# Kernel tuning notes

Hardware: AMD Instinct MI355X
Metric: run time of the kernel (lower is better)

Reference implementation:

```python
import jax, jax.numpy as jnp
import numpy as np

N_NODES = 50000
N_EDGES = 800000
D_IN = 128
D_HID = 128
N_LAYERS = 3
BN_EPS = 1e-5
NEG_SLOPE = 0.2  # GATv2Conv default


def setup_inputs() -> dict:
    key = jax.random.key(0)
    ks = jax.random.split(key, 9)
    x = jax.random.normal(ks[0], (N_NODES, D_IN), dtype=jnp.float32)
    edge_index = jax.random.randint(ks[1], (2, N_EDGES), 0, N_NODES, dtype=jnp.int64)
    s = 1.0 / np.sqrt(D_HID)
    # stacked per-layer params (in_channels == hidden_channels so uniform shapes)
    Wl = jax.random.uniform(ks[2], (N_LAYERS, D_IN, D_HID), jnp.float32, -s, s)   # lin_l (source)
    Wr = jax.random.uniform(ks[3], (N_LAYERS, D_IN, D_HID), jnp.float32, -s, s)   # lin_r (target)
    att = jax.random.uniform(ks[4], (N_LAYERS, D_HID), jnp.float32, -s, s)        # attention vector (heads=1)
    bias = jnp.zeros((N_LAYERS, D_HID), jnp.float32)
    gamma = jnp.ones((N_LAYERS, D_HID), jnp.float32)
    beta = jnp.zeros((N_LAYERS, D_HID), jnp.float32)
    return {"x": x, "edge_index": edge_index, "Wl": Wl, "Wr": Wr, "att": att,
            "bias": bias, "gamma": gamma, "beta": beta}


def reference(x, edge_index, Wl, Wr, att, bias, gamma, beta):
    src = edge_index[0]  # message source j
    dst = edge_index[1]  # message target i
    n = x.shape[0]
    for i in range(N_LAYERS):
        # GATv2Conv, heads=1, add_self_loops=False
        xl = x @ Wl[i]                                   # [N, H] source transform
        xr = x @ Wr[i]                                   # [N, H] target transform
        e = jax.nn.leaky_relu(xl[src] + xr[dst], NEG_SLOPE) @ att[i]  # [E]
        # softmax over incoming edges of each target node
        emax = jax.ops.segment_max(e, dst, num_segments=n)            # [N]
        a = jnp.exp(e - emax[dst])                                    # [E]
        denom = jax.ops.segment_sum(a, dst, num_segments=n)           # [N]
        alpha = a / (denom[dst] + 1e-16)                              # [E]
        out = jax.ops.segment_sum(alpha[:, None] * xl[src], dst, num_segments=n) + bias[i]
        # BatchNorm1d (training-mode batch statistics, biased variance)
        mu = jnp.mean(out, axis=0)
        var = jnp.var(out, axis=0)
        out = gamma[i] * (out - mu) * jax.lax.rsqrt(var + BN_EPS) + beta[i]
        # exact (erf) GELU to match torch F.gelu; dropout p=0.0 -> identity
        x = jax.nn.gelu(out, approximate=False)
    return x
```

## Files before the change

### kernel.cpp

```cpp
#include <hip/hip_runtime.h>
#include <math.h>

#define NNODES 50000
#define NEDGES 800000
#define D 128
#define NEG_SLOPE 0.2f
#define BN_EPS 1e-5f
#define SCAN_THREADS 1024
#define WAVE_REGION 3328
#define COUNTS_PAD (16 * WAVE_REGION)
#define SBIN 4096
#define SUM_SLOTS 64

typedef __attribute__((ext_vector_type(8))) unsigned short ushort8_t;
typedef __attribute__((ext_vector_type(8))) short bf16x8;
typedef __attribute__((ext_vector_type(4))) float f32x4;

__device__ __forceinline__ unsigned short f2bf(float x) {
  unsigned u = __float_as_uint(x);
  u += 0x7fffu + ((u >> 16) & 1u);
  return (unsigned short)(u >> 16);
}
__device__ __forceinline__ float bf2f(unsigned short h) {
  return __uint_as_float((unsigned)h << 16);
}

__global__ __launch_bounds__(256) void k_rank(const int* __restrict__ dst,
        int* __restrict__ counts, int* __restrict__ rank, int E) {
  int e = blockIdx.x * 256 + threadIdx.x;
  if (e < E) rank[e] = atomicAdd(&counts[dst[e]], 1);
}

__global__ __launch_bounds__(1024) void k_scan_sort(const int* __restrict__ counts,
        int* __restrict__ row_ptr, int* __restrict__ node_order, int n) {
  __shared__ int wtot[16];
  __shared__ int hist[SBIN];
  int t = threadIdx.x;
  int lane = t & 63, w = t >> 6;
  int rb = w * WAVE_REGION;
  int tot = 0;
  for (int j = 0; j < 52; ++j) tot += counts[rb + j * 64 + lane];
#pragma unroll
  for (int d = 1; d < 64; d <<= 1) tot += __shfl_xor(tot, d);
  if (lane == 0) wtot[w] = tot;
  __syncthreads();
  int wbase = 0;
#pragma unroll
  for (int i = 0; i < 16; ++i) wbase += (i < w) ? wtot[i] : 0;
  int running = wbase;
  for (int j = 0; j < 52; ++j) {
    int idx = rb + j * 64 + lane;
    int v = counts[idx];
    int incl = v;
#pragma unroll
    for (int d = 1; d < 64; d <<= 1) {
      int u = __shfl_up(incl, d);
      if (lane >= d) incl += u;
    }
    if (idx < n) row_ptr[idx + 1] = running + incl;
    running += __shfl(incl, 63);
  }
  if (t == 0) row_ptr[0] = 0;
  __syncthreads();
  for (int i = t; i < SBIN; i += 1024) hist[i] = 0;
  __syncthreads();
  {
    int k = 0;
    for (int i = t; i < n; i += 1024, ++k) {
      int d = counts[i];
      if (d > 127) d = 127;
      int bin = ((127 - d) << 5) | ((t ^ k) & 31);
      atomicAdd(&hist[bin], 1);
    }
  }
  __syncthreads();
  int b4 = t * 4;
  int h0 = hist[b4], h1 = hist[b4 + 1], h2 = hist[b4 + 2], h3 = hist[b4 + 3];
  int ts = h0 + h1 + h2 + h3;
  int incl = ts;
#pragma unroll
  for (int d = 1; d < 64; d <<= 1) {
    int u = __shfl_up(incl, d);
    if (lane >= d) incl += u;
  }
  if (lane == 63) wtot[w] = incl;
  __syncthreads();
  int wb2 = 0;
#pragma unroll
  for (int i = 0; i < 16; ++i) wb2 += (i < w) ? wtot[i] : 0;
  int ex = wb2 + incl - ts;
  __syncthreads();
  hist[b4]     = ex;
  hist[b4 + 1] = ex + h0;
  hist[b4 + 2] = ex + h0 + h1;
  hist[b4 + 3] = ex + h0 + h1 + h2;
  __syncthreads();
  {
    int k = 0;
    for (int i = t; i < n; i += 1024, ++k) {
      int d = counts[i];
      if (d > 127) d = 127;
      int bin = ((127 - d) << 5) | ((t ^ k) & 31);
      int pos = atomicAdd(&hist[bin], 1);
      node_order[pos] = i;
    }
  }
}

__global__ __launch_bounds__(256) void k_place(const int* __restrict__ src,
        const int* __restrict__ dst, const int* __restrict__ rank,
        const int* __restrict__ row_ptr, int* __restrict__ col_src, int E) {
  int e = blockIdx.x * 256 + threadIdx.x;
  if (e >= E) return;
  col_src[row_ptr[dst[e]] + rank[e]] = src[e];
}

__global__ __launch_bounds__(256) void k_cvt(const float* __restrict__ x,
        const float* __restrict__ Wl, const float* __restrict__ Wr,
        unsigned short* __restrict__ xb, unsigned short* __restrict__ wt,
        int total8) {
  if (blockIdx.x < 6) {
    int ls = blockIdx.x;
    int l = ls >> 1, s = ls & 1;
    const float* W = (s ? Wr : Wl) + l * D * D;
    unsigned short* o = wt + ls * D * D;
    for (int it = 0; it < 64; ++it) {
      int idx = it * 256 + threadIdx.x;
      int k = idx >> 7, c = idx & 127;
      o[c * D + k] = f2bf(W[idx]);
    }
  } else {
    int i = (blockIdx.x - 6) * 256 + threadIdx.x;
    if (i >= total8) return;
    float4 a = ((const float4*)x)[2 * i];
    float4 b = ((const float4*)x)[2 * i + 1];
    uint4 pk;
    pk.x = (unsigned)f2bf(a.x) | ((unsigned)f2bf(a.y) << 16);
    pk.y = (unsigned)f2bf(a.z) | ((unsigned)f2bf(a.w) << 16);
    pk.z = (unsigned)f2bf(b.x) | ((unsigned)f2bf(b.y) << 16);
    pk.w = (unsigned)f2bf(b.z) | ((unsigned)f2bf(b.w) << 16);
    ((uint4*)xb)[i] = pk;
  }
}

__global__ __launch_bounds__(256) void k_gemm(const unsigned short* __restrict__ xb,
        const unsigned short* __restrict__ wt,
        unsigned short* __restrict__ xlb, unsigned short* __restrict__ xrb,
        float* __restrict__ sums64, int n) {
  __shared__ unsigned short xs[128 * 128];
  const int t = threadIdx.x;
  const int row0 = blockIdx.x * 128;
  const unsigned short* __restrict__ W = wt + (size_t)blockIdx.y * (D * D);
  unsigned short* __restrict__ outp = blockIdx.y ? xrb : xlb;

  if (blockIdx.x == 0 && blockIdx.y == 0) {
#pragma unroll
    for (int i = 0; i < SUM_SLOTS; ++i) sums64[i * 256 + t] = 0.f;
  }

#pragma unroll
  for (int i = 0; i < 8; ++i) {
    int ci = i * 256 + t;
    int lr = ci >> 4, p = ci & 15;
    int grow = row0 + lr;
    if (grow >= n) grow = n - 1;
    int gp = p ^ (lr & 7);
    uint4 v = *(const uint4*)(xb + (size_t)grow * D + gp * 8);
    *(uint4*)((char*)xs + ci * 16) = v;
  }
  __syncthreads();

  const int lane = t & 63, wv = t >> 6;
  const int colg = lane & 15, kg = lane >> 4;

  f32x4 acc[2][8];
#pragma unroll
  for (int rr = 0; rr < 2; ++rr)
#pragma unroll
    for (int cc = 0; cc < 8; ++cc) acc[rr][cc] = (f32x4)(0.f);

#pragma unroll
  for (int ks = 0; ks < 4; ++ks) {
    bf16x8 a[2], b[8];
#pragma unroll
    for (int rr = 0; rr < 2; ++rr) {
      int lr = wv * 32 + rr * 16 + colg;
      int byte = (lr * 256 + ks * 64 + kg * 16) ^ ((lr & 7) << 4);
      a[rr] = *(const bf16x8*)((const char*)xs + byte);
    }
#pragma unroll
    for (int cc = 0; cc < 8; ++cc) {
      int col = cc * 16 + colg;
      b[cc] = *(const bf16x8*)(W + (size_t)col * D + ks * 32 + kg * 8);
    }
#pragma unroll
    for (int rr = 0; rr < 2; ++rr)
#pragma unroll
      for (int cc = 0; cc < 8; ++cc)
        acc[rr][cc] = __builtin_amdgcn_mfma_f32_16x16x32_bf16(a[rr], b[cc], acc[rr][cc], 0, 0, 0);
  }

#pragma unroll
  for (int rr = 0; rr < 2; ++rr) {
    int rbase = row0 + wv * 32 + rr * 16 + kg * 4;
#pragma unroll
    for (int cc = 0; cc < 8; ++cc) {
      int col = cc * 16 + colg;
      f32x4 v = acc[rr][cc];
#pragma unroll
      for (int r = 0; r < 4; ++r) {
        int grow = rbase + r;
        if (grow < n) outp[(size_t)grow * D + col] = f2bf(v[r]);
      }
    }
  }
}


__device__ __forceinline__ void agg_step(ushort8_t hv, const float* xrv,
        const float* atv, float& m, float& den, float* ac) {
  float v[8];
#pragma unroll
  for (int j = 0; j < 8; ++j) v[j] = bf2f(hv[j]);
  float p = 0.f;
#pragma unroll
  for (int j = 0; j < 8; ++j) {
    float tt = v[j] + xrv[j];
    tt = tt > 0.f ? tt : NEG_SLOPE * tt;
    p += tt * atv[j];
  }
  p += __shfl_xor(p, 1);
  p += __shfl_xor(p, 2);
  p += __shfl_xor(p, 4);
  p += __shfl_xor(p, 8);
  if (p > m) {
    float sc = __expf(m - p);
    den *= sc;
#pragma unroll
    for (int j = 0; j < 8; ++j) ac[j] *= sc;
    m = p;
  }
  float a = __expf(p - m);
  den += a;
#pragma unroll
  for (int j = 0; j < 8; ++j) ac[j] += a * v[j];
}

__global__ __launch_bounds__(256) void k_agg(const unsigned short* __restrict__ xlb,
        const unsigned short* __restrict__ xrb, const int* __restrict__ col_src,
        const int* __restrict__ row_ptr, const int* __restrict__ node_order,
        const float* __restrict__ att, float* __restrict__ out,
        float* __restrict__ sums64, int n) {
  __shared__ float lsum[16][128];
  __shared__ float lsq[16][128];
  int g = blockIdx.x * 16 + (threadIdx.x >> 4);
  int grp = threadIdx.x >> 4;
  int lane = threadIdx.x & 15;
  bool active = (g < n);
  float r[8];
#pragma unroll
  for (int j = 0; j < 8; ++j) r[j] = 0.f;

  if (active) {
    int node = node_order[g];
    int ro = lane * 2;
    ushort8_t hr = ((const ushort8_t*)(xrb + (size_t)node * D))[lane];
    float xrv[8];
#pragma unroll
    for (int j = 0; j < 8; ++j) xrv[j] = bf2f(hr[j]);
    float4 at0 = ((const float4*)att)[ro];
    float4 at1 = ((const float4*)att)[ro + 1];
    float atv[8] = {at0.x, at0.y, at0.z, at0.w, at1.x, at1.y, at1.z, at1.w};

    int k0 = row_ptr[node], k1 = row_ptr[node + 1];
    float m = -1e30f, den = 0.f;
    float ac[8];
#pragma unroll
    for (int j = 0; j < 8; ++j) ac[j] = 0.f;

    const ushort8_t* xl8 = (const ushort8_t*)xlb;
    int k = k0;
    for (; k + 8 <= k1; k += 8) {
      int s0 = col_src[k],     s1 = col_src[k + 1], s2 = col_src[k + 2], s3 = col_src[k + 3];
      int s4 = col_src[k + 4], s5 = col_src[k + 5], s6 = col_src[k + 6], s7 = col_src[k + 7];
      ushort8_t h0 = xl8[(size_t)s0 * 16 + lane];
      ushort8_t h1 = xl8[(size_t)s1 * 16 + lane];
      ushort8_t h2 = xl8[(size_t)s2 * 16 + lane];
      ushort8_t h3 = xl8[(size_t)s3 * 16 + lane];
      ushort8_t h4 = xl8[(size_t)s4 * 16 + lane];
      ushort8_t h5 = xl8[(size_t)s5 * 16 + lane];
      ushort8_t h6 = xl8[(size_t)s6 * 16 + lane];
      ushort8_t h7 = xl8[(size_t)s7 * 16 + lane];
      agg_step(h0, xrv, atv, m, den, ac);
      agg_step(h1, xrv, atv, m, den, ac);
      agg_step(h2, xrv, atv, m, den, ac);
      agg_step(h3, xrv, atv, m, den, ac);
      agg_step(h4, xrv, atv, m, den, ac);
      agg_step(h5, xrv, atv, m, den, ac);
      agg_step(h6, xrv, atv, m, den, ac);
      agg_step(h7, xrv, atv, m, den, ac);
    }
    if (k + 4 <= k1) {
      int s0 = col_src[k], s1 = col_src[k + 1], s2 = col_src[k + 2], s3 = col_src[k + 3];
      ushort8_t h0 = xl8[(size_t)s0 * 16 + lane];
      ushort8_t h1 = xl8[(size_t)s1 * 16 + lane];
      ushort8_t h2 = xl8[(size_t)s2 * 16 + lane];
      ushort8_t h3 = xl8[(size_t)s3 * 16 + lane];
      agg_step(h0, xrv, atv, m, den, ac);
      agg_step(h1, xrv, atv, m, den, ac);
      agg_step(h2, xrv, atv, m, den, ac);
      agg_step(h3, xrv, atv, m, den, ac);
      k += 4;
    }
    for (; k < k1; ++k) {
      int s = col_src[k];
      ushort8_t h = xl8[(size_t)s * 16 + lane];
      agg_step(h, xrv, atv, m, den, ac);
    }

    float inv = 1.f / (den + 1e-16f);
#pragma unroll
    for (int j = 0; j < 8; ++j) r[j] = ac[j] * inv;
    float4* o4 = (float4*)out;
    o4[(size_t)node * 32 + ro]     = make_float4(r[0], r[1], r[2], r[3]);
    o4[(size_t)node * 32 + ro + 1] = make_float4(r[4], r[5], r[6], r[7]);
  }

#pragma unroll
  for (int j = 0; j < 8; ++j) {
    lsum[grp][lane * 8 + j] = r[j];
    lsq[grp][lane * 8 + j] = r[j] * r[j];
  }
  __syncthreads();
  int t = threadIdx.x;
  float s = 0.f;
  if (t < 128) {
#pragma unroll
    for (int gg = 0; gg < 16; ++gg) s += lsum[gg][t];
  } else {
#pragma unroll
    for (int gg = 0; gg < 16; ++gg) s += lsq[gg][t - 128];
  }
  atomicAdd(&sums64[(blockIdx.x & (SUM_SLOTS - 1)) * 256 + t], s);
}

__global__ void k_bn_fin2(const float* __restrict__ sums64,
        const float* __restrict__ gamma, const float* __restrict__ beta,
        float* __restrict__ ss, float inv_n) {
  __shared__ float tot[256];
  int t = threadIdx.x;
  float a0 = 0.f, a1 = 0.f, a2 = 0.f, a3 = 0.f;
#pragma unroll
  for (int k = 0; k < SUM_SLOTS; k += 4) {
    a0 += sums64[(k + 0) * 256 + t];
    a1 += sums64[(k + 1) * 256 + t];
    a2 += sums64[(k + 2) * 256 + t];
    a3 += sums64[(k + 3) * 256 + t];
  }
  tot[t] = (a0 + a1) + (a2 + a3);
  __syncthreads();
  if (t < 128) {
    float mu = tot[t] * inv_n;
    float var = tot[128 + t] * inv_n - mu * mu;
    float rs = rsqrtf(var + BN_EPS);
    float sc = gamma[t] * rs;
    ss[t] = sc;
    ss[128 + t] = beta[t] - mu * sc;
  }
}

__global__ __launch_bounds__(256) void k_bn_apply(const float* __restrict__ agg,
        const float* __restrict__ ss, float* __restrict__ xo,
        unsigned short* __restrict__ xbo, int total4, int last) {
  int i = blockIdx.x * 256 + threadIdx.x;
  if (i >= total4) return;
  float4 v = ((const float4*)agg)[i];
  int c4 = i & (D / 4 - 1);
  float4 sc = ((const float4*)ss)[c4];
  float4 sh = ((const float4*)ss)[D / 4 + c4];
  float y0 = sc.x * v.x + sh.x;
  float y1 = sc.y * v.y + sh.y;
  float y2 = sc.z * v.z + sh.z;
  float y3 = sc.w * v.w + sh.w;
  float4 g;
  g.x = 0.5f * y0 * (1.f + erff(y0 * 0.70710678118654752f));
  g.y = 0.5f * y1 * (1.f + erff(y1 * 0.70710678118654752f));
  g.z = 0.5f * y2 * (1.f + erff(y2 * 0.70710678118654752f));
  g.w = 0.5f * y3 * (1.f + erff(y3 * 0.70710678118654752f));
  if (last) {
    ((float4*)xo)[i] = g;
  } else {
    uint2 pk;
    pk.x = (unsigned)f2bf(g.x) | ((unsigned)f2bf(g.y) << 16);
    pk.y = (unsigned)f2bf(g.z) | ((unsigned)f2bf(g.w) << 16);
    ((uint2*)xbo)[i] = pk;
  }
}


extern "C" void kernel_launch(void* const* d_in, const int* in_sizes, int n_in,
                              void* d_out, int out_size, void* d_ws, size_t ws_size,
                              hipStream_t stream) {
  const float* x0    = (const float*)d_in[0];
  const int*   ei    = (const int*)d_in[1];
  const float* Wl    = (const float*)d_in[2];
  const float* Wr    = (const float*)d_in[3];
  const float* att   = (const float*)d_in[4];
  const float* gamma = (const float*)d_in[6];
  const float* beta  = (const float*)d_in[7];
  float* out = (float*)d_out;

  float* ws = (float*)d_ws;
  unsigned short* xb  = (unsigned short*)ws;
  unsigned short* xlb = (unsigned short*)(ws + 3200000);
  unsigned short* xrb = (unsigned short*)(ws + 6400000);
  int*   col_src    = (int*)(ws + 9600000);
  int*   rank       = (int*)(ws + 10400000);
  int*   row_ptr    = (int*)(ws + 11200000);
  int*   counts     = (int*)(ws + 11250004);
  int*   node_order = (int*)(ws + 11303252);
  float* sums64     = ws + 11353252;
  float* ss         = ws + 11369636;
  unsigned short* wt = (unsigned short*)(ws + 11369892);

  const int* src = ei;
  const int* dst = ei + NEDGES;

  hipMemsetAsync(counts, 0, COUNTS_PAD * sizeof(int), stream);
  k_rank<<<(NEDGES + 255) / 256, 256, 0, stream>>>(dst, counts, rank, NEDGES);
  k_scan_sort<<<1, SCAN_THREADS, 0, stream>>>(counts, row_ptr, node_order, NNODES);
  k_place<<<(NEDGES + 255) / 256, 256, 0, stream>>>(src, dst, rank, row_ptr, col_src, NEDGES);
  k_cvt<<<6 + (NNODES * (D / 8) + 255) / 256, 256, 0, stream>>>(x0, Wl, Wr, xb, wt,
                                                                NNODES * (D / 8));

  dim3 ggrid((NNODES + 127) / 128, 2);

  for (int l = 0; l < 3; ++l) {
    k_gemm<<<ggrid, 256, 0, stream>>>(xb, wt + (size_t)l * 2 * D * D, xlb, xrb,
                                      sums64, NNODES);

    k_agg<<<(NNODES + 15) / 16, 256, 0, stream>>>(xlb, xrb, col_src, row_ptr,
                                                  node_order, att + l * D, out,
                                                  sums64, NNODES);

    k_bn_fin2<<<1, 256, 0, stream>>>(sums64, gamma + l * D, beta + l * D, ss, 1.0f / NNODES);
    k_bn_apply<<<(NNODES * (D / 4) + 255) / 256, 256, 0, stream>>>(out, ss, out, xb,
                                                                   NNODES * (D / 4),
                                                                   l == 2 ? 1 : 0);
  }
}
```

Before: 355.3 us.

## Move degree-sort histogram and placement out of single-block scan into grid kernels

The degree-bucket counting sort of nodes used to run inside the single 1024-thread scan block, looping twice over all 50k nodes with shared-memory atomics. It now runs as two grid-wide kernels: one builds a global histogram and one places nodes. The scan block only reads 8 bins per thread and writes prefix cursors. This removes serial work from one workgroup, at the cost of two extra launches and global atomics.

Result: no change. 350.9 us (-1.2%).

```diff
diff --git a/kernel.cpp b/kernel.cpp
--- a/kernel.cpp
+++ b/kernel.cpp
@@ -9,7 +9,8 @@
 #define SCAN_THREADS 1024
 #define WAVE_REGION 3328
 #define COUNTS_PAD (16 * WAVE_REGION)
-#define SBIN 4096
+#define DSUB 64
+#define DBINS (128 * DSUB)
 #define SUM_SLOTS 64
 
 typedef __attribute__((ext_vector_type(8))) unsigned short ushort8_t;
@@ -31,10 +32,19 @@
   if (e < E) rank[e] = atomicAdd(&counts[dst[e]], 1);
 }
 
+__global__ __launch_bounds__(256) void k_deg_hist(const int* __restrict__ counts,
+        int* __restrict__ dhist, int n) {
+  int i = blockIdx.x * 256 + threadIdx.x;
+  if (i >= n) return;
+  int d = counts[i];
+  if (d > 127) d = 127;
+  atomicAdd(&dhist[((127 - d) << 6) | (i & (DSUB - 1))], 1);
+}
+
 __global__ __launch_bounds__(1024) void k_scan_sort(const int* __restrict__ counts,
-        int* __restrict__ row_ptr, int* __restrict__ node_order, int n) {
+        const int* __restrict__ dhist, int* __restrict__ row_ptr,
+        int* __restrict__ dcur, int n) {
   __shared__ int wtot[16];
-  __shared__ int hist[SBIN];
   int t = threadIdx.x;
   int lane = t & 63, w = t >> 6;
   int rb = w * WAVE_REGION;
@@ -62,21 +72,11 @@
   }
   if (t == 0) row_ptr[0] = 0;
   __syncthreads();
-  for (int i = t; i < SBIN; i += 1024) hist[i] = 0;
-  __syncthreads();
-  {
-    int k = 0;
-    for (int i = t; i < n; i += 1024, ++k) {
-      int d = counts[i];
-      if (d > 127) d = 127;
-      int bin = ((127 - d) << 5) | ((t ^ k) & 31);
-      atomicAdd(&hist[bin], 1);
-    }
-  }
-  __syncthreads();
-  int b4 = t * 4;
-  int h0 = hist[b4], h1 = hist[b4 + 1], h2 = hist[b4 + 2], h3 = hist[b4 + 3];
-  int ts = h0 + h1 + h2 + h3;
+  int b8 = t * 8;
+  int h[8];
+  int ts = 0;
+#pragma unroll
+  for (int j = 0; j < 8; ++j) { h[j] = dhist[b8 + j]; ts += h[j]; }
   int incl = ts;
 #pragma unroll
   for (int d = 1; d < 64; d <<= 1) {
@@ -89,22 +89,18 @@
 #pragma unroll
   for (int i = 0; i < 16; ++i) wb2 += (i < w) ? wtot[i] : 0;
   int ex = wb2 + incl - ts;
-  __syncthreads();
-  hist[b4]     = ex;
-  hist[b4 + 1] = ex + h0;
-  hist[b4 + 2] = ex + h0 + h1;
-  hist[b4 + 3] = ex + h0 + h1 + h2;
-  __syncthreads();
-  {
-    int k = 0;
-    for (int i = t; i < n; i += 1024, ++k) {
-      int d = counts[i];
-      if (d > 127) d = 127;
-      int bin = ((127 - d) << 5) | ((t ^ k) & 31);
-      int pos = atomicAdd(&hist[bin], 1);
-      node_order[pos] = i;
-    }
-  }
+#pragma unroll
+  for (int j = 0; j < 8; ++j) { dcur[b8 + j] = ex; ex += h[j]; }
+}
+
+__global__ __launch_bounds__(256) void k_deg_place(const int* __restrict__ counts,
+        int* __restrict__ dcur, int* __restrict__ node_order, int n) {
+  int i = blockIdx.x * 256 + threadIdx.x;
+  if (i >= n) return;
+  int d = counts[i];
+  if (d > 127) d = 127;
+  int pos = atomicAdd(&dcur[((127 - d) << 6) | (i & (DSUB - 1))], 1);
+  node_order[pos] = i;
 }
 
 __global__ __launch_bounds__(256) void k_place(const int* __restrict__ src,
@@ -418,17 +414,21 @@
   int*   rank       = (int*)(ws + 10400000);
   int*   row_ptr    = (int*)(ws + 11200000);
   int*   counts     = (int*)(ws + 11250004);
-  int*   node_order = (int*)(ws + 11303252);
-  float* sums64     = ws + 11353252;
-  float* ss         = ws + 11369636;
-  unsigned short* wt = (unsigned short*)(ws + 11369892);
+  int*   dhist      = (int*)(ws + 11303252);
+  int*   dcur       = (int*)(ws + 11311444);
+  int*   node_order = (int*)(ws + 11319636);
+  float* sums64     = ws + 11369636;
+  float* ss         = ws + 11386020;
+  unsigned short* wt = (unsigned short*)(ws + 11386276);
 
   const int* src = ei;
   const int* dst = ei + NEDGES;
 
-  hipMemsetAsync(counts, 0, COUNTS_PAD * sizeof(int), stream);
+  hipMemsetAsync(counts, 0, (COUNTS_PAD + DBINS) * sizeof(int), stream);
   k_rank<<<(NEDGES + 255) / 256, 256, 0, stream>>>(dst, counts, rank, NEDGES);
-  k_scan_sort<<<1, SCAN_THREADS, 0, stream>>>(counts, row_ptr, node_order, NNODES);
+  k_deg_hist<<<(NNODES + 255) / 256, 256, 0, stream>>>(counts, dhist, NNODES);
+  k_scan_sort<<<1, SCAN_THREADS, 0, stream>>>(counts, dhist, row_ptr, dcur, NNODES);
+  k_deg_place<<<(NNODES + 255) / 256, 256, 0, stream>>>(counts, dcur, node_order, NNODES);
   k_place<<<(NEDGES + 255) / 256, 256, 0, stream>>>(src, dst, rank, row_ptr, col_src, NEDGES);
   k_cvt<<<6 + (NNODES * (D / 8) + 255) / 256, 256, 0, stream>>>(x0, Wl, Wr, xb, wt,
                                                                 NNODES * (D / 8));
```
